# Kernel optimization log

Hardware: AMD Instinct MI355X
Metric: run time of the kernel (lower is better)

Reference implementation:

```python
import jax, jax.numpy as jnp
import numpy as np

N_NODES = 50000
N_EDGES = 800000
D_IN = 128
D_H = 128
D_OUT = 2
N_GRAPHS = 512
EPS = 1e-5


def _sage(x, src, dst, Wl, bl, Wr):
    # mean aggregation of source features at destination nodes
    msum = jax.ops.segment_sum(x[src], dst, num_segments=N_NODES)
    deg = jax.ops.segment_sum(jnp.ones((src.shape[0],), x.dtype), dst, num_segments=N_NODES)
    agg = msum / jnp.clip(deg, 1.0)[:, None]
    return agg @ Wl.T + bl + x @ Wr.T


def _bn(x, g, b, m, v):
    return (x - m) * jax.lax.rsqrt(v + EPS) * g + b


def setup_inputs() -> dict:
    key = jax.random.key(0)
    ks = jax.random.split(key, 24)
    s = lambda k, shape, fan: (jax.random.normal(k, shape, jnp.float32) / np.sqrt(fan))
    x = jax.random.normal(ks[0], (N_NODES, D_IN), jnp.float32)
    edge_index = jax.random.randint(ks[1], (2, N_EDGES), 0, N_NODES, jnp.int64)
    batch = jnp.sort(jax.random.randint(ks[2], (N_NODES,), 0, N_GRAPHS, jnp.int64))
    inp = {"x": x, "edge_index": edge_index, "batch": batch}
    # SAGEConv layers: lin_l (with bias) on aggregated, lin_r (no bias) on root
    dims = [(D_IN, D_H), (D_H, D_H), (D_H, D_OUT)]
    for i, (di, do) in enumerate(dims):
        inp[f"Wl{i}"] = s(ks[3 + 3 * i], (do, di), di)
        inp[f"bl{i}"] = jnp.zeros((do,), jnp.float32)
        inp[f"Wr{i}"] = s(ks[4 + 3 * i], (do, di), di)
    # BatchNorm (eval mode: running stats)
    for i in range(2):
        inp[f"g{i}"] = jnp.ones((D_H,), jnp.float32)
        inp[f"b{i}"] = jnp.zeros((D_H,), jnp.float32)
        inp[f"m{i}"] = 0.1 * jax.random.normal(ks[12 + 2 * i], (D_H,), jnp.float32)
        inp[f"v{i}"] = jax.random.uniform(ks[13 + 2 * i], (D_H,), jnp.float32, 0.5, 1.5)
    # graph prediction MLP: Linear(2*D_OUT, D_H) -> ReLU -> Linear(D_H, D_OUT)
    inp["mW1"] = s(ks[20], (D_H, 2 * D_OUT), 2 * D_OUT)
    inp["mb1"] = jnp.zeros((D_H,), jnp.float32)
    inp["mW2"] = s(ks[21], (D_OUT, D_H), D_H)
    inp["mb2"] = jnp.zeros((D_OUT,), jnp.float32)
    return inp


def reference(x, edge_index, batch, Wl0, bl0, Wr0, Wl1, bl1, Wr1, Wl2, bl2, Wr2,
              g0, b0, m0, v0, g1, b1, m1, v1, mW1, mb1, mW2, mb2):
    src, dst = edge_index[0], edge_index[1]
    h = _sage(x, src, dst, Wl0, bl0, Wr0)
    h = jax.nn.relu(_bn(h, g0, b0, m0, v0))  # dropout inactive in eval
    h = _sage(h, src, dst, Wl1, bl1, Wr1)
    h = jax.nn.relu(_bn(h, g1, b1, m1, v1))
    h = _sage(h, src, dst, Wl2, bl2, Wr2)  # [N, D_OUT]
    # global mean + max pooling per graph
    cnt = jax.ops.segment_sum(jnp.ones((h.shape[0],), h.dtype), batch, num_segments=N_GRAPHS)
    pmean = jax.ops.segment_sum(h, batch, num_segments=N_GRAPHS) / jnp.clip(cnt, 1.0)[:, None]
    pmax = jax.ops.segment_max(h, batch, num_segments=N_GRAPHS)
    g = jnp.concatenate([pmean, pmax], axis=1)  # [G, 2*D_OUT]
    g = jax.nn.relu(g @ mW1.T + mb1)
    return g @ mW2.T + mb2  # [G, D_OUT]
```

## Files before the change

### kernel.cpp

```cpp
#include <hip/hip_runtime.h>
#include <hip/hip_bf16.h>
#include <float.h>

#define N_NODES 50000
#define N_EDGES 800000
#define D_H 128
#define N_GRAPHS 512
#define EPSV 1e-5f
#define NB_SCAN ((N_NODES + 255) / 256)

__device__ __forceinline__ void atomicMaxF(float* addr, float val) {
    if (val >= 0.0f) atomicMax((int*)addr, __float_as_int(val));
    else atomicMin((unsigned int*)addr, (unsigned int)__float_as_int(val));
}

__global__ void hist_kernel(const int* __restrict__ dst, int* __restrict__ cnt) {
    int e = blockIdx.x * blockDim.x + threadIdx.x;
    if (e < N_EDGES) atomicAdd(&cnt[dst[e]], 1);
}

__global__ __launch_bounds__(256) void scan_local_kernel(const int* __restrict__ cnt,
                                                         int* __restrict__ row_ptr,
                                                         int* __restrict__ bsum) {
    __shared__ int sh[256];
    int t = threadIdx.x;
    int i = blockIdx.x * 256 + t;
    int v = (i < N_NODES) ? cnt[i] : 0;
    sh[t] = v;
    __syncthreads();
    int x = v;
    for (int off = 1; off < 256; off <<= 1) {
        int y = (t >= off) ? sh[t - off] : 0;
        __syncthreads();
        x += y;
        sh[t] = x;
        __syncthreads();
    }
    if (i < N_NODES) row_ptr[i] = x - v;
    if (t == 255) bsum[blockIdx.x] = x;
}

__global__ __launch_bounds__(256) void scan_bsum_kernel(const int* __restrict__ bsum,
                                                        int* __restrict__ bofs) {
    __shared__ int sh[256];
    int t = threadIdx.x;
    int v = (t < NB_SCAN) ? bsum[t] : 0;
    sh[t] = v;
    __syncthreads();
    int x = v;
    for (int off = 1; off < 256; off <<= 1) {
        int y = (t >= off) ? sh[t - off] : 0;
        __syncthreads();
        x += y;
        sh[t] = x;
        __syncthreads();
    }
    if (t < NB_SCAN) bofs[t] = x - v;
}

__global__ __launch_bounds__(256) void scan_add_kernel(int* __restrict__ row_ptr,
                                                       int* __restrict__ wofs,
                                                       const int* __restrict__ bofs,
                                                       float* __restrict__ psum,
                                                       float* __restrict__ pcnt,
                                                       float* __restrict__ pmax) {
    int t = threadIdx.x;
    int i = blockIdx.x * 256 + t;
    if (i < N_NODES) {
        int r = row_ptr[i] + bofs[blockIdx.x];
        row_ptr[i] = r;
        wofs[i] = r;
    }
    if (i == 0) row_ptr[N_NODES] = N_EDGES;
    if (i < N_GRAPHS * 2) { psum[i] = 0.f; pmax[i] = -FLT_MAX; }
    if (i < N_GRAPHS) pcnt[i] = 0.f;
}

__global__ void scatter_kernel(const int* __restrict__ src, const int* __restrict__ dst,
                               int* __restrict__ wofs, int* __restrict__ csr_src) {
    int e = blockIdx.x * blockDim.x + threadIdx.x;
    if (e < N_EDGES) {
        int pos = atomicAdd(&wofs[dst[e]], 1);
        csr_src[pos] = src[e];
    }
}

#define ROWS 32
#define RPW 8
template <int MODE>
__global__ __launch_bounds__(256, 4) void fused_sage_kernel(
    const float* __restrict__ xin,
    const int* __restrict__ row_ptr, const int* __restrict__ csr_src,
    const float* __restrict__ Wl, const float* __restrict__ bl,
    const float* __restrict__ Wr,
    const float* __restrict__ gg, const float* __restrict__ bb,
    const float* __restrict__ mm, const float* __restrict__ vv,
    float* __restrict__ hout,
    const float* __restrict__ Wl2, const float* __restrict__ Wr2,
    float* __restrict__ p2r2) {
    __shared__ float s_agg[ROWS][D_H];
    __shared__ float s_x[ROWS][D_H];
    int row0 = blockIdx.x * ROWS;
    int t = threadIdx.x;
    int lane = t & 63;
    int w = t >> 6;

    for (int idx = t; idx < ROWS * (D_H / 4); idx += 256) {
        int r = idx >> 5;
        int c4 = idx & 31;
        int row = row0 + r;
        float4 vx = make_float4(0, 0, 0, 0);
        if (row < N_NODES) vx = ((const float4*)(xin + (size_t)row * D_H))[c4];
        ((float4*)s_x[r])[c4] = vx;
    }

    const float2* xp = (const float2*)xin;
    for (int rr = 0; rr < RPW; rr++) {
        int r = w * RPW + rr;
        int row = row0 + r;
        float ax = 0.f, ay = 0.f;
        if (row < N_NODES) {
            int s0 = row_ptr[row], s1 = row_ptr[row + 1];
            int e = s0;
            for (; e + 3 < s1; e += 4) {
                int sa = csr_src[e], sb = csr_src[e + 1];
                int sc = csr_src[e + 2], sd = csr_src[e + 3];
                float2 va = xp[(size_t)sa * 64 + lane];
                float2 vb = xp[(size_t)sb * 64 + lane];
                float2 vc = xp[(size_t)sc * 64 + lane];
                float2 vd = xp[(size_t)sd * 64 + lane];
                ax += (va.x + vb.x) + (vc.x + vd.x);
                ay += (va.y + vb.y) + (vc.y + vd.y);
            }
            for (; e < s1; e++) {
                float2 va = xp[(size_t)csr_src[e] * 64 + lane];
                ax += va.x;
                ay += va.y;
            }
            float inv = 1.0f / (float)max(s1 - s0, 1);
            ax *= inv;
            ay *= inv;
        }
        ((float2*)s_agg[r])[lane] = make_float2(ax, ay);
    }
    __syncthreads();

    int j = lane;
    int rg = w;
    const float4* wl0 = (const float4*)(Wl + (size_t)j * D_H);
    const float4* wl1 = (const float4*)(Wl + (size_t)(j + 64) * D_H);
    const float4* wr0 = (const float4*)(Wr + (size_t)j * D_H);
    const float4* wr1 = (const float4*)(Wr + (size_t)(j + 64) * D_H);

    float acc0[RPW], acc1[RPW];
#pragma unroll
    for (int r = 0; r < RPW; r++) { acc0[r] = 0.f; acc1[r] = 0.f; }

    for (int k0 = 0; k0 < D_H / 4; k0 += 2) {
        float4 a0[2], a1[2], b0[2], b1[2];
#pragma unroll
        for (int q = 0; q < 2; q++) {
            a0[q] = wl0[k0 + q];
            a1[q] = wl1[k0 + q];
            b0[q] = wr0[k0 + q];
            b1[q] = wr1[k0 + q];
        }
#pragma unroll
        for (int r = 0; r < RPW; r++) {
            int row = rg * RPW + r;
#pragma unroll
            for (int q = 0; q < 2; q++) {
                float4 xa = ((const float4*)s_agg[row])[k0 + q];
                float4 xx = ((const float4*)s_x[row])[k0 + q];
                acc0[r] += xa.x * a0[q].x + xa.y * a0[q].y + xa.z * a0[q].z + xa.w * a0[q].w
                         + xx.x * b0[q].x + xx.y * b0[q].y + xx.z * b0[q].z + xx.w * b0[q].w;
                acc1[r] += xa.x * a1[q].x + xa.y * a1[q].y + xa.z * a1[q].z + xa.w * a1[q].w
                         + xx.x * b1[q].x + xx.y * b1[q].y + xx.z * b1[q].z + xx.w * b1[q].w;
            }
        }
    }

    float sc0 = gg[j] * rsqrtf(vv[j] + EPSV);
    float sh0 = bb[j] + (bl[j] - mm[j]) * sc0;
    float sc1 = gg[j + 64] * rsqrtf(vv[j + 64] + EPSV);
    float sh1 = bb[j + 64] + (bl[j + 64] - mm[j + 64]) * sc1;

    if (MODE == 0) {
#pragma unroll
        for (int r = 0; r < RPW; r++) {
            int row = row0 + rg * RPW + r;
            if (row < N_NODES) {
                hout[(size_t)row * D_H + j] = fmaxf(acc0[r] * sc0 + sh0, 0.f);
                hout[(size_t)row * D_H + j + 64] = fmaxf(acc1[r] * sc1 + sh1, 0.f);
            }
        }
    } else {
        float wl2_0a = Wl2[j],       wl2_0b = Wl2[j + 64];
        float wl2_1a = Wl2[128 + j], wl2_1b = Wl2[192 + j];
        float wr2_0a = Wr2[j],       wr2_0b = Wr2[j + 64];
        float wr2_1a = Wr2[128 + j], wr2_1b = Wr2[192 + j];
#pragma unroll
        for (int r = 0; r < RPW; r++) {
            float v0 = fmaxf(acc0[r] * sc0 + sh0, 0.f);
            float v1 = fmaxf(acc1[r] * sc1 + sh1, 0.f);
            float p0 = v0 * wl2_0a + v1 * wl2_0b;
            float p1 = v0 * wl2_1a + v1 * wl2_1b;
            float p2 = v0 * wr2_0a + v1 * wr2_0b;
            float p3 = v0 * wr2_1a + v1 * wr2_1b;
            for (int off = 32; off; off >>= 1) {
                p0 += __shfl_down(p0, off);
                p1 += __shfl_down(p1, off);
                p2 += __shfl_down(p2, off);
                p3 += __shfl_down(p3, off);
            }
            int row = row0 + rg * RPW + r;
            if (lane == 0 && row < N_NODES)
                ((float4*)p2r2)[row] = make_float4(p0, p1, p2, p3);
        }
    }
}

__global__ __launch_bounds__(256) void aggpool_kernel(
    const float* __restrict__ p2r2, const int* __restrict__ row_ptr,
    const int* __restrict__ csr_src, const int* __restrict__ batch,
    const float* __restrict__ bl2,
    float* __restrict__ psum, float* __restrict__ pcnt, float* __restrict__ pmax) {
    int i = blockIdx.x * blockDim.x + threadIdx.x;
    if (i >= N_NODES) return;
    int s0 = row_ptr[i], s1 = row_ptr[i + 1];
    float a0 = 0.f, a1 = 0.f;
    int e = s0;
    for (; e + 3 < s1; e += 4) {
        float2 v0 = ((const float2*)p2r2)[(size_t)csr_src[e] * 2];
        float2 v1 = ((const float2*)p2r2)[(size_t)csr_src[e + 1] * 2];
        float2 v2 = ((const float2*)p2r2)[(size_t)csr_src[e + 2] * 2];
        float2 v3 = ((const float2*)p2r2)[(size_t)csr_src[e + 3] * 2];
        a0 += (v0.x + v1.x) + (v2.x + v3.x);
        a1 += (v0.y + v1.y) + (v2.y + v3.y);
    }
    for (; e < s1; e++) {
        float2 v = ((const float2*)p2r2)[(size_t)csr_src[e] * 2];
        a0 += v.x;
        a1 += v.y;
    }
    float inv = 1.0f / (float)max(s1 - s0, 1);
    float2 r = ((const float2*)p2r2)[(size_t)i * 2 + 1];
    float h0 = a0 * inv + bl2[0] + r.x;
    float h1 = a1 * inv + bl2[1] + r.y;
    int b = batch[i];
    atomicAdd(&psum[b * 2], h0);
    atomicAdd(&psum[b * 2 + 1], h1);
    atomicAdd(&pcnt[b], 1.0f);
    atomicMaxF(&pmax[b * 2], h0);
    atomicMaxF(&pmax[b * 2 + 1], h1);
}

__global__ __launch_bounds__(128) void mlp_kernel(
    const float* __restrict__ psum, const float* __restrict__ pcnt,
    const float* __restrict__ pmax,
    const float* __restrict__ mW1, const float* __restrict__ mb1,
    const float* __restrict__ mW2, const float* __restrict__ mb2,
    float* __restrict__ out) {
    int b = blockIdx.x;
    int t = threadIdx.x;
    float cntv = fmaxf(pcnt[b], 1.0f);
    float g0 = psum[b * 2] / cntv;
    float g1 = psum[b * 2 + 1] / cntv;
    float g2 = pmax[b * 2];
    float g3 = pmax[b * 2 + 1];
    float4 w = ((const float4*)mW1)[t];
    float h = fmaxf(g0 * w.x + g1 * w.y + g2 * w.z + g3 * w.w + mb1[t], 0.f);
    float o0 = h * mW2[t];
    float o1 = h * mW2[128 + t];
    for (int off = 32; off; off >>= 1) {
        o0 += __shfl_down(o0, off);
        o1 += __shfl_down(o1, off);
    }
    __shared__ float sh[4];
    if ((t & 63) == 0) {
        sh[(t >> 6) * 2] = o0;
        sh[(t >> 6) * 2 + 1] = o1;
    }
    __syncthreads();
    if (t == 0) {
        out[b * 2] = sh[0] + sh[2] + mb2[0];
        out[b * 2 + 1] = sh[1] + sh[3] + mb2[1];
    }
}

extern "C" void kernel_launch(void* const* d_in, const int* in_sizes, int n_in,
                              void* d_out, int out_size, void* d_ws, size_t ws_size,
                              hipStream_t stream) {
    const float* x = (const float*)d_in[0];
    const int* ei = (const int*)d_in[1];
    const int* batch = (const int*)d_in[2];
    const float* Wl0 = (const float*)d_in[3];
    const float* bl0 = (const float*)d_in[4];
    const float* Wr0 = (const float*)d_in[5];
    const float* Wl1 = (const float*)d_in[6];
    const float* bl1 = (const float*)d_in[7];
    const float* Wr1 = (const float*)d_in[8];
    const float* Wl2 = (const float*)d_in[9];
    const float* bl2 = (const float*)d_in[10];
    const float* Wr2 = (const float*)d_in[11];
    const float* g0 = (const float*)d_in[12];
    const float* b0 = (const float*)d_in[13];
    const float* m0 = (const float*)d_in[14];
    const float* v0 = (const float*)d_in[15];
    const float* g1 = (const float*)d_in[16];
    const float* b1 = (const float*)d_in[17];
    const float* m1 = (const float*)d_in[18];
    const float* v1 = (const float*)d_in[19];
    const float* mW1 = (const float*)d_in[20];
    const float* mb1 = (const float*)d_in[21];
    const float* mW2 = (const float*)d_in[22];
    const float* mb2 = (const float*)d_in[23];

    const int* src = ei;
    const int* dst = ei + N_EDGES;

    char* ws = (char*)d_ws;
    size_t off = 0;
    auto alloc = [&](size_t bytes) -> char* {
        char* p = ws + off;
        off += (bytes + 255) & ~(size_t)255;
        return p;
    };
    int* cnt = (int*)alloc((size_t)N_NODES * 4);
    int* row_ptr = (int*)alloc((size_t)(N_NODES + 1) * 4);
    int* wofs = (int*)alloc((size_t)N_NODES * 4);
    int* csr_src = (int*)alloc((size_t)N_EDGES * 4);
    float* h0 = (float*)alloc((size_t)N_NODES * D_H * 4);
    float* p2r2 = (float*)alloc((size_t)N_NODES * 16);
    float* psum = (float*)alloc((size_t)N_GRAPHS * 2 * 4);
    float* pcnt = (float*)alloc((size_t)N_GRAPHS * 4);
    float* pmax = (float*)alloc((size_t)N_GRAPHS * 2 * 4);
    int* bsum = (int*)alloc((size_t)NB_SCAN * 4);
    int* bofs = (int*)alloc((size_t)NB_SCAN * 4);
    (void)ws_size;

    hipMemsetAsync(cnt, 0, (size_t)N_NODES * 4, stream);
    hist_kernel<<<(N_EDGES + 255) / 256, 256, 0, stream>>>(dst, cnt);
    scan_local_kernel<<<NB_SCAN, 256, 0, stream>>>(cnt, row_ptr, bsum);
    scan_bsum_kernel<<<1, 256, 0, stream>>>(bsum, bofs);
    scan_add_kernel<<<NB_SCAN, 256, 0, stream>>>(row_ptr, wofs, bofs, psum, pcnt, pmax);
    scatter_kernel<<<(N_EDGES + 255) / 256, 256, 0, stream>>>(src, dst, wofs, csr_src);

    int nblk = (N_NODES + ROWS - 1) / ROWS;

    fused_sage_kernel<0><<<nblk, 256, 0, stream>>>(
        x, row_ptr, csr_src, Wl0, bl0, Wr0, g0, b0, m0, v0, h0,
        nullptr, nullptr, nullptr);

    fused_sage_kernel<1><<<nblk, 256, 0, stream>>>(
        h0, row_ptr, csr_src, Wl1, bl1, Wr1, g1, b1, m1, v1, nullptr,
        Wl2, Wr2, p2r2);

    aggpool_kernel<<<(N_NODES + 255) / 256, 256, 0, stream>>>(
        p2r2, row_ptr, csr_src, batch, bl2, psum, pcnt, pmax);

    mlp_kernel<<<N_GRAPHS, 128, 0, stream>>>(psum, pcnt, pmax, mW1, mb1, mW2, mb2,
                                             (float*)d_out);
}
```

Baseline: 672.1 us.

## Use 8 waves per block, scalarize neighbor indices, drop block barrier

The fused SAGE kernel now runs 512 threads (8 waves, 4 rows each) per 32-row block instead of 256 threads with 8 rows each. This doubles the waves available to hide gather latency. Neighbor indices are made wave-uniform with readfirstlane, the gather loop is unrolled by 8 with 2- and 1-edge tails, and each wave loads its own root rows. Because each wave only touches its own shared-memory rows, the block-wide barrier is removed. The larger blocks and unroll may raise register pressure against the requested occupancy, and the Wl/Wr weights are now read by twice as many waves per block.

```diff
diff --git a/kernel.cpp b/kernel.cpp
--- a/kernel.cpp
+++ b/kernel.cpp
@@ -86,9 +86,10 @@
 }
 
 #define ROWS 32
-#define RPW 8
+#define WAVES 8
+#define RPW 4
 template <int MODE>
-__global__ __launch_bounds__(256, 4) void fused_sage_kernel(
+__global__ __launch_bounds__(512, 6) void fused_sage_kernel(
     const float* __restrict__ xin,
     const int* __restrict__ row_ptr, const int* __restrict__ csr_src,
     const float* __restrict__ Wl, const float* __restrict__ bl,
@@ -105,48 +106,60 @@
     int lane = t & 63;
     int w = t >> 6;
 
-    for (int idx = t; idx < ROWS * (D_H / 4); idx += 256) {
-        int r = idx >> 5;
-        int c4 = idx & 31;
-        int row = row0 + r;
-        float4 vx = make_float4(0, 0, 0, 0);
-        if (row < N_NODES) vx = ((const float4*)(xin + (size_t)row * D_H))[c4];
-        ((float4*)s_x[r])[c4] = vx;
-    }
-
     const float2* xp = (const float2*)xin;
+
     for (int rr = 0; rr < RPW; rr++) {
         int r = w * RPW + rr;
         int row = row0 + r;
+        float2 vx = make_float2(0.f, 0.f);
         float ax = 0.f, ay = 0.f;
         if (row < N_NODES) {
+            vx = xp[(size_t)row * 64 + lane];
             int s0 = row_ptr[row], s1 = row_ptr[row + 1];
             int e = s0;
-            for (; e + 3 < s1; e += 4) {
-                int sa = csr_src[e], sb = csr_src[e + 1];
-                int sc = csr_src[e + 2], sd = csr_src[e + 3];
-                float2 va = xp[(size_t)sa * 64 + lane];
-                float2 vb = xp[(size_t)sb * 64 + lane];
-                float2 vc = xp[(size_t)sc * 64 + lane];
-                float2 vd = xp[(size_t)sd * 64 + lane];
-                ax += (va.x + vb.x) + (vc.x + vd.x);
-                ay += (va.y + vb.y) + (vc.y + vd.y);
-            }
-            for (; e < s1; e++) {
-                float2 va = xp[(size_t)csr_src[e] * 64 + lane];
-                ax += va.x;
-                ay += va.y;
+            for (; e + 7 < s1; e += 8) {
+                int i0 = __builtin_amdgcn_readfirstlane(csr_src[e]);
+                int i1 = __builtin_amdgcn_readfirstlane(csr_src[e + 1]);
+                int i2 = __builtin_amdgcn_readfirstlane(csr_src[e + 2]);
+                int i3 = __builtin_amdgcn_readfirstlane(csr_src[e + 3]);
+                int i4 = __builtin_amdgcn_readfirstlane(csr_src[e + 4]);
+                int i5 = __builtin_amdgcn_readfirstlane(csr_src[e + 5]);
+                int i6 = __builtin_amdgcn_readfirstlane(csr_src[e + 6]);
+                int i7 = __builtin_amdgcn_readfirstlane(csr_src[e + 7]);
+                float2 v0 = xp[(size_t)i0 * 64 + lane];
+                float2 v1 = xp[(size_t)i1 * 64 + lane];
+                float2 v2 = xp[(size_t)i2 * 64 + lane];
+                float2 v3 = xp[(size_t)i3 * 64 + lane];
+                float2 v4 = xp[(size_t)i4 * 64 + lane];
+                float2 v5 = xp[(size_t)i5 * 64 + lane];
+                float2 v6 = xp[(size_t)i6 * 64 + lane];
+                float2 v7 = xp[(size_t)i7 * 64 + lane];
+                ax += ((v0.x + v1.x) + (v2.x + v3.x)) + ((v4.x + v5.x) + (v6.x + v7.x));
+                ay += ((v0.y + v1.y) + (v2.y + v3.y)) + ((v4.y + v5.y) + (v6.y + v7.y));
+            }
+            for (; e + 1 < s1; e += 2) {
+                int i0 = __builtin_amdgcn_readfirstlane(csr_src[e]);
+                int i1 = __builtin_amdgcn_readfirstlane(csr_src[e + 1]);
+                float2 v0 = xp[(size_t)i0 * 64 + lane];
+                float2 v1 = xp[(size_t)i1 * 64 + lane];
+                ax += v0.x + v1.x;
+                ay += v0.y + v1.y;
+            }
+            if (e < s1) {
+                int i0 = __builtin_amdgcn_readfirstlane(csr_src[e]);
+                float2 v0 = xp[(size_t)i0 * 64 + lane];
+                ax += v0.x;
+                ay += v0.y;
             }
             float inv = 1.0f / (float)max(s1 - s0, 1);
             ax *= inv;
             ay *= inv;
         }
+        ((float2*)s_x[r])[lane] = vx;
         ((float2*)s_agg[r])[lane] = make_float2(ax, ay);
     }
-    __syncthreads();
 
     int j = lane;
-    int rg = w;
     const float4* wl0 = (const float4*)(Wl + (size_t)j * D_H);
     const float4* wl1 = (const float4*)(Wl + (size_t)(j + 64) * D_H);
     const float4* wr0 = (const float4*)(Wr + (size_t)j * D_H);
@@ -167,7 +180,7 @@
         }
 #pragma unroll
         for (int r = 0; r < RPW; r++) {
-            int row = rg * RPW + r;
+            int row = w * RPW + r;
 #pragma unroll
             for (int q = 0; q < 2; q++) {
                 float4 xa = ((const float4*)s_agg[row])[k0 + q];
@@ -188,7 +201,7 @@
     if (MODE == 0) {
 #pragma unroll
         for (int r = 0; r < RPW; r++) {
-            int row = row0 + rg * RPW + r;
+            int row = row0 + w * RPW + r;
             if (row < N_NODES) {
                 hout[(size_t)row * D_H + j] = fmaxf(acc0[r] * sc0 + sh0, 0.f);
                 hout[(size_t)row * D_H + j + 64] = fmaxf(acc1[r] * sc1 + sh1, 0.f);
@@ -213,7 +226,7 @@
                 p2 += __shfl_down(p2, off);
                 p3 += __shfl_down(p3, off);
             }
-            int row = row0 + rg * RPW + r;
+            int row = row0 + w * RPW + r;
             if (lane == 0 && row < N_NODES)
                 ((float4*)p2r2)[row] = make_float4(p0, p1, p2, p3);
         }
@@ -348,11 +361,11 @@
 
     int nblk = (N_NODES + ROWS - 1) / ROWS;
 
-    fused_sage_kernel<0><<<nblk, 256, 0, stream>>>(
+    fused_sage_kernel<0><<<nblk, 512, 0, stream>>>(
         x, row_ptr, csr_src, Wl0, bl0, Wr0, g0, b0, m0, v0, h0,
         nullptr, nullptr, nullptr);
 
-    fused_sage_kernel<1><<<nblk, 256, 0, stream>>>(
+    fused_sage_kernel<1><<<nblk, 512, 0, stream>>>(
         h0, row_ptr, csr_src, Wl1, bl1, Wr1, g1, b1, m1, v1, nullptr,
         Wl2, Wr2, p2r2);
 
```

Result: slower. 1.493 ms (+122.2%).

## Balance edge gathering across warps with packed CSR and LDS atomics

Applied to the files above, without the earlier changes.

Each CSR entry now packs the source index with the low 5 bits of the destination row, so a block can split its contiguous edge range evenly over its four waves instead of giving each wave a fixed set of rows. Each wave gathers neighbor features in double-buffered batches of 8 and accumulates them into shared memory with atomic adds; the mean division happens afterward. This targets load imbalance from uneven per-row degrees and raises memory-level parallelism. In exchange it adds LDS atomic contention and an extra synchronisation. The pooling kernel is updated to unpack the source index.

```diff
diff --git a/kernel.cpp b/kernel.cpp
--- a/kernel.cpp
+++ b/kernel.cpp
@@ -80,8 +80,9 @@
                                int* __restrict__ wofs, int* __restrict__ csr_src) {
     int e = blockIdx.x * blockDim.x + threadIdx.x;
     if (e < N_EDGES) {
-        int pos = atomicAdd(&wofs[dst[e]], 1);
-        csr_src[pos] = src[e];
+        int d = dst[e];
+        int pos = atomicAdd(&wofs[d], 1);
+        csr_src[pos] = (src[e] << 5) | (d & 31);
     }
 }
 
@@ -105,48 +106,77 @@
     int lane = t & 63;
     int w = t >> 6;
 
+    const float2* xp = (const float2*)xin;
+
+    float4 z4 = make_float4(0.f, 0.f, 0.f, 0.f);
     for (int idx = t; idx < ROWS * (D_H / 4); idx += 256) {
+        ((float4*)s_agg)[idx] = z4;
         int r = idx >> 5;
         int c4 = idx & 31;
         int row = row0 + r;
-        float4 vx = make_float4(0, 0, 0, 0);
+        float4 vx = z4;
         if (row < N_NODES) vx = ((const float4*)(xin + (size_t)row * D_H))[c4];
         ((float4*)s_x[r])[c4] = vx;
     }
-
-    const float2* xp = (const float2*)xin;
+    __syncthreads();
+
+    int E0 = row_ptr[row0];
+    int rend = row0 + ROWS; if (rend > N_NODES) rend = N_NODES;
+    int E1 = row_ptr[rend];
+    int len = E1 - E0;
+    int per = (len + 3) >> 2;
+    int es = E0 + w * per; if (es > E1) es = E1;
+    int ee = es + per;     if (ee > E1) ee = E1;
+
+    int sA[8]; float2 vA[8];
+    int sB[8]; float2 vB[8];
+    auto loadC = [&](int* S, float2* V, int eb) {
+#pragma unroll
+        for (int i = 0; i < 8; i++) S[i] = csr_src[eb + i];
+#pragma unroll
+        for (int i = 0; i < 8; i++) V[i] = xp[(size_t)(S[i] >> 5) * 64 + lane];
+    };
+    auto commitC = [&](const int* S, const float2* V) {
+#pragma unroll
+        for (int i = 0; i < 8; i++) {
+            int dl = S[i] & 31;
+            atomicAdd(&s_agg[dl][lane * 2], V[i].x);
+            atomicAdd(&s_agg[dl][lane * 2 + 1], V[i].y);
+        }
+    };
+
+    int e = es;
+    int nfull = (ee - es) >> 3;
+    if (nfull > 0) {
+        loadC(sA, vA, e); e += 8;
+        for (int c = 1; c < nfull; c++) {
+            if (c & 1) { loadC(sB, vB, e); commitC(sA, vA); }
+            else       { loadC(sA, vA, e); commitC(sB, vB); }
+            e += 8;
+        }
+        if (nfull & 1) commitC(sA, vA); else commitC(sB, vB);
+    }
+    for (; e < ee; e++) {
+        int pk = csr_src[e];
+        float2 v = xp[(size_t)(pk >> 5) * 64 + lane];
+        atomicAdd(&s_agg[pk & 31][lane * 2], v.x);
+        atomicAdd(&s_agg[pk & 31][lane * 2 + 1], v.y);
+    }
+    __syncthreads();
+
+#pragma unroll
     for (int rr = 0; rr < RPW; rr++) {
         int r = w * RPW + rr;
         int row = row0 + r;
-        float ax = 0.f, ay = 0.f;
         if (row < N_NODES) {
-            int s0 = row_ptr[row], s1 = row_ptr[row + 1];
-            int e = s0;
-            for (; e + 3 < s1; e += 4) {
-                int sa = csr_src[e], sb = csr_src[e + 1];
-                int sc = csr_src[e + 2], sd = csr_src[e + 3];
-                float2 va = xp[(size_t)sa * 64 + lane];
-                float2 vb = xp[(size_t)sb * 64 + lane];
-                float2 vc = xp[(size_t)sc * 64 + lane];
-                float2 vd = xp[(size_t)sd * 64 + lane];
-                ax += (va.x + vb.x) + (vc.x + vd.x);
-                ay += (va.y + vb.y) + (vc.y + vd.y);
-            }
-            for (; e < s1; e++) {
-                float2 va = xp[(size_t)csr_src[e] * 64 + lane];
-                ax += va.x;
-                ay += va.y;
-            }
-            float inv = 1.0f / (float)max(s1 - s0, 1);
-            ax *= inv;
-            ay *= inv;
-        }
-        ((float2*)s_agg[r])[lane] = make_float2(ax, ay);
-    }
-    __syncthreads();
+            int deg = row_ptr[row + 1] - row_ptr[row];
+            float inv = 1.0f / (float)max(deg, 1);
+            float2 v = ((float2*)s_agg[r])[lane];
+            ((float2*)s_agg[r])[lane] = make_float2(v.x * inv, v.y * inv);
+        }
+    }
 
     int j = lane;
-    int rg = w;
     const float4* wl0 = (const float4*)(Wl + (size_t)j * D_H);
     const float4* wl1 = (const float4*)(Wl + (size_t)(j + 64) * D_H);
     const float4* wr0 = (const float4*)(Wr + (size_t)j * D_H);
@@ -167,7 +197,7 @@
         }
 #pragma unroll
         for (int r = 0; r < RPW; r++) {
-            int row = rg * RPW + r;
+            int row = w * RPW + r;
 #pragma unroll
             for (int q = 0; q < 2; q++) {
                 float4 xa = ((const float4*)s_agg[row])[k0 + q];
@@ -188,7 +218,7 @@
     if (MODE == 0) {
 #pragma unroll
         for (int r = 0; r < RPW; r++) {
-            int row = row0 + rg * RPW + r;
+            int row = row0 + w * RPW + r;
             if (row < N_NODES) {
                 hout[(size_t)row * D_H + j] = fmaxf(acc0[r] * sc0 + sh0, 0.f);
                 hout[(size_t)row * D_H + j + 64] = fmaxf(acc1[r] * sc1 + sh1, 0.f);
@@ -213,7 +243,7 @@
                 p2 += __shfl_down(p2, off);
                 p3 += __shfl_down(p3, off);
             }
-            int row = row0 + rg * RPW + r;
+            int row = row0 + w * RPW + r;
             if (lane == 0 && row < N_NODES)
                 ((float4*)p2r2)[row] = make_float4(p0, p1, p2, p3);
         }
@@ -231,15 +261,15 @@
     float a0 = 0.f, a1 = 0.f;
     int e = s0;
     for (; e + 3 < s1; e += 4) {
-        float2 v0 = ((const float2*)p2r2)[(size_t)csr_src[e] * 2];
-        float2 v1 = ((const float2*)p2r2)[(size_t)csr_src[e + 1] * 2];
-        float2 v2 = ((const float2*)p2r2)[(size_t)csr_src[e + 2] * 2];
-        float2 v3 = ((const float2*)p2r2)[(size_t)csr_src[e + 3] * 2];
+        float2 v0 = ((const float2*)p2r2)[(size_t)(csr_src[e] >> 5) * 2];
+        float2 v1 = ((const float2*)p2r2)[(size_t)(csr_src[e + 1] >> 5) * 2];
+        float2 v2 = ((const float2*)p2r2)[(size_t)(csr_src[e + 2] >> 5) * 2];
+        float2 v3 = ((const float2*)p2r2)[(size_t)(csr_src[e + 3] >> 5) * 2];
         a0 += (v0.x + v1.x) + (v2.x + v3.x);
         a1 += (v0.y + v1.y) + (v2.y + v3.y);
     }
     for (; e < s1; e++) {
-        float2 v = ((const float2*)p2r2)[(size_t)csr_src[e] * 2];
+        float2 v = ((const float2*)p2r2)[(size_t)(csr_src[e] >> 5) * 2];
         a0 += v.x;
         a1 += v.y;
     }
```

After: 1.584 ms. 136% more time.
